# Kernel optimization log

Measured on AMD Instinct MI355X. Metric: run time of the kernel, lower is better.

Reference implementation:

```python
import jax, jax.numpy as jnp
import numpy as np

H, Dh, D = 12, 64, 8          # heads, head dim, depth slices
DS = Dh // D                   # per-depth slice dim = 8
EPS = 1e-6
MAW_STRENGTH = 0.15
ALPHA = 1.0 + 10.0 * MAW_STRENGTH  # 2.5


def _min_max_norm(v, eps=1e-12):
    vmin = v.min(axis=-1, keepdims=True)
    vmax = v.max(axis=-1, keepdims=True)
    return (v - vmin) / jnp.maximum(vmax - vmin, eps)


def setup_inputs() -> dict:
    key = jax.random.key(0)
    ks = jax.random.split(key, 8)
    B, L, E = 2, 768, H * Dh
    s = 0.02
    return {
        "hidden_states": jax.random.normal(ks[0], (B, L, E), jnp.float32),
        "attention_mask": jnp.zeros((B, L), jnp.float32),  # additive mask
        "Wq": jax.random.normal(ks[1], (E, E), jnp.float32) * s,
        "bq": jnp.zeros((E,), jnp.float32),
        "Wk": jax.random.normal(ks[2], (E, E), jnp.float32) * s,
        "bk": jnp.zeros((E,), jnp.float32),
        "Wv": jax.random.normal(ks[3], (E, E), jnp.float32) * s,
        "bv": jnp.zeros((E,), jnp.float32),
    }


def reference(hidden_states, attention_mask, Wq, bq, Wk, bk, Wv, bv):
    B, L, E = hidden_states.shape
    # projections -> [B, H, L, Dh]
    q = (hidden_states @ Wq + bq).reshape(B, L, H, Dh).transpose(0, 2, 1, 3)
    k = (hidden_states @ Wk + bk).reshape(B, L, H, Dh).transpose(0, 2, 1, 3)
    v = (hidden_states @ Wv + bv).reshape(B, L, H, Dh).transpose(0, 2, 1, 3)

    # depth-wise expansion: split head dim into D slices of size DS
    qd = q.reshape(B, H, L, D, DS)
    kd = k.reshape(B, H, L, D, DS)
    scores = jnp.einsum("bhqds,bhkds->bhdqk", qd, kd) / jnp.sqrt(jnp.float32(DS))
    # additive mask [B, Lk] -> [B, 1, 1, 1, Lk]
    scores = scores + attention_mask[:, None, None, None, :]
    attn = jax.nn.softmax(scores, axis=-1)  # [B, H, D, Lq, Lk]

    # statistical depth gating (mode='stat')
    var_k = jnp.var(attn, axis=-1, ddof=1).mean(axis=(1, 3))          # [B, D]
    max_k = attn.max(axis=-1).mean(axis=(1, 3))                        # [B, D]
    p = jnp.clip(attn, EPS, None)
    ent = (-p * jnp.log(p)).sum(axis=-1).mean(axis=(1, 3))             # [B, D]
    hhi = (attn * attn).sum(axis=-1).mean(axis=(1, 3))                 # [B, D]

    score = (0.5 * _min_max_norm(var_k) + 0.3 * _min_max_norm(max_k)
             + 0.2 * _min_max_norm(hhi) - 0.4 * _min_max_norm(ent))
    weights = jax.nn.softmax(ALPHA * score, axis=-1)                   # [B, D]

    # depth compression -> [B, H, Lq, Lk]
    attn4 = jnp.einsum("bhdqk,bd->bhqk", attn, weights)
    ctx = jnp.einsum("bhqk,bhkd->bhqd", attn4, v)                      # [B, H, L, Dh]
    ctx = ctx.transpose(0, 2, 1, 3).reshape(B, L, H * Dh)
    return ctx, attn4
```

## Files before the change

kernel.cpp:

```cpp
#include <hip/hip_runtime.h>

#define BATCH 2
#define L_SEQ 768
#define NH 12
#define DH 64
#define ND 8
#define EMB 768
#define RSQRT8 0.35355339059327373f

#define OFF_Q    0
#define OFF_K    1179648
#define OFF_V    2359296
#define OFF_L    3538944
#define OFF_PART 3686400
#define OFF_P2   6045696
#define OFF_W    6046464

__global__ __launch_bounds__(256) void k1_qkv(
    const float* __restrict__ hs,
    const float* __restrict__ Wq, const float* __restrict__ bq,
    const float* __restrict__ Wk, const float* __restrict__ bk,
    const float* __restrict__ Wv, const float* __restrict__ bvp,
    float* __restrict__ qw, float* __restrict__ kw, float* __restrict__ vw)
{
    __shared__ float AsT[64][68];
    __shared__ float Bs[64][68];
    const int tid = threadIdx.x;
    const int tx = tid & 15, ty = tid >> 4;
    const int bx = blockIdx.x, by = blockIdx.y, gz = blockIdx.z;
    const float* W    = (gz == 0) ? Wq : (gz == 1 ? Wk : Wv);
    const float* bias = (gz == 0) ? bq : (gz == 1 ? bk : bvp);
    float* dst        = (gz == 0) ? qw : (gz == 1 ? kw : vw);

    const int ldc = tx * 4;

    float acc[4][4];
#pragma unroll
    for (int i = 0; i < 4; i++)
#pragma unroll
        for (int j = 0; j < 4; j++) acc[i][j] = 0.f;

    for (int k0 = 0; k0 < EMB; k0 += 64) {
        __syncthreads();
#pragma unroll
        for (int i = 0; i < 4; i++) {
            int r = ty + 16 * i;
            float4 a = *(const float4*)&hs[(size_t)(by * 64 + r) * EMB + k0 + ldc];
            AsT[ldc + 0][r] = a.x; AsT[ldc + 1][r] = a.y;
            AsT[ldc + 2][r] = a.z; AsT[ldc + 3][r] = a.w;
            *(float4*)&Bs[r][ldc] =
                *(const float4*)&W[(size_t)(k0 + r) * EMB + bx * 64 + ldc];
        }
        __syncthreads();
#pragma unroll 8
        for (int kk = 0; kk < 64; kk++) {
            float av[4], bb[4];
            *(float4*)av = *(const float4*)&AsT[kk][ty * 4];
            *(float4*)bb = *(const float4*)&Bs[kk][tx * 4];
#pragma unroll
            for (int i = 0; i < 4; i++)
#pragma unroll
                for (int j = 0; j < 4; j++)
                    acc[i][j] = fmaf(av[i], bb[j], acc[i][j]);
        }
    }

#pragma unroll
    for (int i = 0; i < 4; i++) {
        int m = by * 64 + ty * 4 + i;
        int b2 = m / L_SEQ, l = m % L_SEQ;
        float o[4];
#pragma unroll
        for (int j = 0; j < 4; j++) o[j] = acc[i][j] + bias[bx * 64 + tx * 4 + j];
        *(float4*)&dst[((size_t)(b2 * NH + bx) * L_SEQ + l) * DH + tx * 4] = *(float4*)o;
    }
}

__global__ __launch_bounds__(256) void k2_stats(
    const float* __restrict__ qw, const float* __restrict__ kw,
    const float* __restrict__ mask, float* __restrict__ part)
{
    __shared__ float k_lds[64 * 64];
    __shared__ float m_lds[64];
    const int tid = threadIdx.x;
    const int lane = tid & 63, w = tid >> 6;
    const int qr = lane >> 3, d = lane & 7;
    const int lb = (blockIdx.x & 7) * 144 + (blockIdx.x >> 3);
    const int kq = lb & 3;
    const int t2 = lb >> 2;
    const int bh = t2 / 12;
    const int q0 = (t2 % 12) * 64;
    const int b = bh / NH;
    const int qw0 = q0 + w * 16;

    float qf[2][8];
#pragma unroll
    for (int qq = 0; qq < 2; qq++) {
        const float* qp = &qw[((size_t)bh * L_SEQ + qw0 + qr + qq * 8) * DH + d * 8];
        *(float4*)&qf[qq][0] = *(const float4*)qp;
        *(float4*)&qf[qq][4] = *(const float4*)(qp + 4);
    }
    float S[2] = {0.f, 0.f}, T2[2] = {0.f, 0.f}, SL[2] = {0.f, 0.f};
    float M[2] = {-1e30f, -1e30f};

    const int kb0 = kq * 192;
    for (int c = 0; c < 3; c++) {
        const int kb = kb0 + c * 64;
        __syncthreads();
        {
            const float* src = &kw[((size_t)bh * L_SEQ + kb) * DH];
#pragma unroll
            for (int i = 0; i < 4; i++) {
                int f = tid + 256 * i;
                *(float4*)&k_lds[f * 4] = *(const float4*)&src[f * 4];
            }
            if (tid < 64) m_lds[tid] = mask[b * L_SEQ + kb + tid];
        }
        __syncthreads();
#pragma unroll 4
        for (int kk = 0; kk < 64; kk++) {
            float kv[8];
            *(float4*)&kv[0] = *(const float4*)&k_lds[kk * 64 + d * 8];
            *(float4*)&kv[4] = *(const float4*)&k_lds[kk * 64 + d * 8 + 4];
            float mval = m_lds[kk];
#pragma unroll
            for (int qq = 0; qq < 2; qq++) {
                float s = 0.f;
#pragma unroll
                for (int t = 0; t < 8; t++) s = fmaf(qf[qq][t], kv[t], s);
                s = fmaf(s, RSQRT8, mval);
                float e = __expf(s);
                S[qq] += e;
                T2[qq] = fmaf(e, e, T2[qq]);
                SL[qq] = fmaf(s, e, SL[qq]);
                M[qq] = fmaxf(M[qq], s);
            }
        }
    }
#pragma unroll
    for (int qq = 0; qq < 2; qq++) {
        int q = qw0 + qr + qq * 8;
        size_t base = (size_t)(bh * 8 + d) * 16;
        part[(base + 0 + kq) * 768 + q] = S[qq];
        part[(base + 4 + kq) * 768 + q] = T2[qq];
        part[(base + 8 + kq) * 768 + q] = SL[qq];
        part[(base + 12 + kq) * 768 + q] = M[qq];
    }
}

__global__ __launch_bounds__(256) void k3_reduce(
    const float* __restrict__ part, float* __restrict__ linv,
    float* __restrict__ part2)
{
    const int bdh = blockIdx.x;
    const int bd = bdh / 12, h = bdh % 12;
    const int b = bd >> 3, d = bd & 7;
    const int bh = b * NH + h;
    const int tid = threadIdx.x;
    const int lane = tid & 63, wave = tid >> 6;
    const size_t base = (size_t)(bh * 8 + d) * 16;
    float acc[4] = {0.f, 0.f, 0.f, 0.f};

    for (int q = tid; q < 768; q += 256) {
        float Sv = 0.f, T2v = 0.f, SLv = 0.f, Mv = -1e30f;
#pragma unroll
        for (int kq = 0; kq < 4; kq++) {
            Sv  += part[(base + 0 + kq) * 768 + q];
            T2v += part[(base + 4 + kq) * 768 + q];
            SLv += part[(base + 8 + kq) * 768 + q];
            Mv = fmaxf(Mv, part[(base + 12 + kq) * 768 + q]);
        }
        float inv = 1.0f / Sv;
        linv[((size_t)bh * 768 + q) * 8 + d] = inv;
        float hhi = T2v * inv * inv;
        float maxp = __expf(Mv) * inv;
        float ent = __logf(Sv) - SLv * inv;
        float var = (hhi - (1.0f / 768.0f)) * (1.0f / 767.0f);
        acc[0] += var; acc[1] += maxp; acc[2] += ent; acc[3] += hhi;
    }
    __shared__ float red[4][4];
#pragma unroll
    for (int st = 0; st < 4; st++) {
        float a = acc[st];
#pragma unroll
        for (int off = 32; off > 0; off >>= 1) a += __shfl_xor(a, off, 64);
        acc[st] = a;
    }
    if (lane == 0) {
#pragma unroll
        for (int st = 0; st < 4; st++) red[wave][st] = acc[st];
    }
    __syncthreads();
    if (tid == 0) {
#pragma unroll
        for (int st = 0; st < 4; st++)
            part2[(size_t)(bd * 12 + h) * 4 + st] =
                red[0][st] + red[1][st] + red[2][st] + red[3][st];
    }
}

__global__ __launch_bounds__(64) void k3_weights(
    const float* __restrict__ part2, float* __restrict__ wgt)
{
    __shared__ float stats_l[64];
    const int tid = threadIdx.x;
    {
        const int bd = tid >> 2, st = tid & 3;
        float s = 0.f;
#pragma unroll
        for (int h = 0; h < 12; h++) s += part2[(size_t)(bd * 12 + h) * 4 + st];
        stats_l[tid] = s * (1.0f / 9216.0f);
    }
    __syncthreads();
    if (tid == 0) {
        for (int b = 0; b < BATCH; b++) {
            float v[4][8];
            for (int st = 0; st < 4; st++)
                for (int d = 0; d < 8; d++) v[st][d] = stats_l[(b * 8 + d) * 4 + st];
            float nrm[4][8];
            for (int st = 0; st < 4; st++) {
                float mn = v[st][0], mx = v[st][0];
                for (int d = 1; d < 8; d++) { mn = fminf(mn, v[st][d]); mx = fmaxf(mx, v[st][d]); }
                float rng = fmaxf(mx - mn, 1e-12f);
                for (int d = 0; d < 8; d++) nrm[st][d] = (v[st][d] - mn) / rng;
            }
            float sc[8];
            for (int d = 0; d < 8; d++)
                sc[d] = 0.5f * nrm[0][d] + 0.3f * nrm[1][d] + 0.2f * nrm[3][d] - 0.4f * nrm[2][d];
            float m = 2.5f * sc[0];
            for (int d = 1; d < 8; d++) m = fmaxf(m, 2.5f * sc[d]);
            float e8[8]; float ssum = 0.f;
            for (int d = 0; d < 8; d++) { e8[d] = __expf(2.5f * sc[d] - m); ssum += e8[d]; }
            for (int d = 0; d < 8; d++) wgt[b * ND + d] = e8[d] / ssum;
        }
    }
}

__global__ __launch_bounds__(256, 4) void k45_fused(
    const float* __restrict__ qw, const float* __restrict__ kw,
    const float* __restrict__ vw, const float* __restrict__ mask,
    const float* __restrict__ linv, const float* __restrict__ wgt,
    float* __restrict__ out_a4, float* __restrict__ out_ctx)
{
    __shared__ float smem[4][64 * 20];
    const int tid = threadIdx.x;
    const int lane = tid & 63, w = tid >> 6;
    const int lb = (blockIdx.x & 7) * 144 + (blockIdx.x >> 3);
    const int bh = lb / 48;
    const int q0 = (lb % 48) * 16;
    const int b = bh / NH, h = bh % NH;
    const int qg = lane >> 4;
    const int dhl = lane & 15;

    const float* kbase = &kw[(size_t)bh * L_SEQ * DH];
    const float* vbase = &vw[(size_t)bh * L_SEQ * DH];
    const float* qtile = &qw[((size_t)bh * L_SEQ + q0) * DH];
    const float* ltile = &linv[((size_t)bh * L_SEQ + q0) * 8];

    float wv[8];
#pragma unroll
    for (int d = 0; d < 8; d++) wv[d] = wgt[b * ND + d];

    float acc[4][4];
#pragma unroll
    for (int i = 0; i < 4; i++)
#pragma unroll
        for (int j = 0; j < 4; j++) acc[i][j] = 0.f;

    float* sm = &smem[w][0];

    for (int c = 0; c < 3; c++) {
        const int kb = (w * 3 + c) * 64;
        const int krow = kb + lane;

        float kv[64];
        {
            const float* kp = &kbase[(size_t)krow * DH];
#pragma unroll
            for (int t = 0; t < 16; t++)
                *(float4*)&kv[t * 4] = *(const float4*)&kp[t * 4];
        }
        const float mval = mask[b * L_SEQ + krow];

#pragma unroll 2
        for (int q = 0; q < 16; q++) {
            const float* qp = &qtile[(size_t)q * DH];
            const float* lp = &ltile[(size_t)q * 8];
            float sd[8];
#pragma unroll
            for (int d = 0; d < 8; d++) sd[d] = 0.f;
#pragma unroll
            for (int d = 0; d < 8; d++)
#pragma unroll
                for (int t = 0; t < 8; t++)
                    sd[d] = fmaf(qp[d * 8 + t], kv[d * 8 + t], sd[d]);
            float a4v = 0.f;
#pragma unroll
            for (int d = 0; d < 8; d++) {
                float sv = fmaf(sd[d], RSQRT8, mval);
                a4v = fmaf(wv[d] * lp[d], __expf(sv), a4v);
            }
            out_a4[((size_t)bh * L_SEQ + q0 + q) * L_SEQ + krow] = a4v;
            sm[lane * 20 + q] = a4v;
        }

        const float* vrow = &vbase[(size_t)kb * DH + dhl * 4];
#pragma unroll 8
        for (int k = 0; k < 64; k++) {
            float av[4];
            *(float4*)av = *(const float4*)&sm[k * 20 + qg * 4];
            float4 vv = *(const float4*)&vrow[(size_t)k * DH];
#pragma unroll
            for (int i = 0; i < 4; i++) {
                acc[i][0] = fmaf(av[i], vv.x, acc[i][0]);
                acc[i][1] = fmaf(av[i], vv.y, acc[i][1]);
                acc[i][2] = fmaf(av[i], vv.z, acc[i][2]);
                acc[i][3] = fmaf(av[i], vv.w, acc[i][3]);
            }
        }
    }

#pragma unroll
    for (int i = 0; i < 4; i++)
        *(float4*)&sm[(qg * 4 + i) * 68 + dhl * 4] = *(float4*)&acc[i][0];
    __syncthreads();
    {
        const int q = tid >> 4;
        const int dh4 = (tid & 15) * 4;
        float r[4] = {0.f, 0.f, 0.f, 0.f};
#pragma unroll
        for (int ww = 0; ww < 4; ww++) {
            const float* s2 = &smem[ww][q * 68 + dh4];
#pragma unroll
            for (int j = 0; j < 4; j++) r[j] += s2[j];
        }
        *(float4*)&out_ctx[((size_t)b * L_SEQ + q0 + q) * EMB + h * DH + dh4] =
            *(float4*)r;
    }
}

extern "C" void kernel_launch(void* const* d_in, const int* in_sizes, int n_in,
                              void* d_out, int out_size, void* d_ws, size_t ws_size,
                              hipStream_t stream)
{
    const float* hs   = (const float*)d_in[0];
    const float* mask = (const float*)d_in[1];
    const float* Wq   = (const float*)d_in[2];
    const float* bq   = (const float*)d_in[3];
    const float* Wk   = (const float*)d_in[4];
    const float* bk   = (const float*)d_in[5];
    const float* Wv   = (const float*)d_in[6];
    const float* bv   = (const float*)d_in[7];

    float* ws = (float*)d_ws;
    float* qw    = ws + OFF_Q;
    float* kw    = ws + OFF_K;
    float* vw    = ws + OFF_V;
    float* linv  = ws + OFF_L;
    float* part  = ws + OFF_PART;
    float* part2 = ws + OFF_P2;
    float* wgt   = ws + OFF_W;

    float* out_ctx = (float*)d_out;
    float* out_a4  = (float*)d_out + (size_t)BATCH * L_SEQ * EMB;

    k1_qkv<<<dim3(12, 24, 3), 256, 0, stream>>>(hs, Wq, bq, Wk, bk, Wv, bv, qw, kw, vw);
    k2_stats<<<dim3(1152), 256, 0, stream>>>(qw, kw, mask, part);
    k3_reduce<<<dim3(192), 256, 0, stream>>>(part, linv, part2);
    k3_weights<<<dim3(1), 64, 0, stream>>>(part2, wgt);
    k45_fused<<<dim3(1152), 256, 0, stream>>>(qw, kw, vw, mask, linv, wgt,
                                              out_a4, out_ctx);
}
```

Before: 317.3 us.

## Rewrite QKV GEMM with register-held rows and prefetch K tiles in stats kernel

The QKV projection kernel drops its LDS-tiled 64x64 GEMM. Instead, each lane holds one hidden-state row chunk of 64 floats in registers and reads 8 weight columns per wave as wave-uniform scalar loads. The launch becomes a 1D grid of 1728 blocks with an XCD-aware block remap, intended to avoid LDS traffic and barriers. The stats kernel now register-prefetches the next K tile and mask chunk while the current tile is computed, overlapping global loads with math. The tradeoff is heavy register pressure from the 64-float kv array, plus lower reuse because each block covers only 32 output columns, which raises global and scalar load traffic on the weights.

```diff
diff --git a/kernel.cpp b/kernel.cpp
--- a/kernel.cpp
+++ b/kernel.cpp
@@ -16,64 +16,59 @@
 #define OFF_P2   6045696
 #define OFF_W    6046464
 
-__global__ __launch_bounds__(256) void k1_qkv(
+__global__ __launch_bounds__(256, 4) void k1_qkv(
     const float* __restrict__ hs,
     const float* __restrict__ Wq, const float* __restrict__ bq,
     const float* __restrict__ Wk, const float* __restrict__ bk,
     const float* __restrict__ Wv, const float* __restrict__ bvp,
     float* __restrict__ qw, float* __restrict__ kw, float* __restrict__ vw)
 {
-    __shared__ float AsT[64][68];
-    __shared__ float Bs[64][68];
-    const int tid = threadIdx.x;
-    const int tx = tid & 15, ty = tid >> 4;
-    const int bx = blockIdx.x, by = blockIdx.y, gz = blockIdx.z;
+    const int tid = threadIdx.x;
+    const int lane = tid & 63;
+    const int lb = (blockIdx.x & 7) * 216 + (blockIdx.x >> 3);
+    const int gz = lb / 576;
+    const int r2 = lb % 576;
+    const int by = r2 / 24;
+    const int bx = r2 % 24;
+
     const float* W    = (gz == 0) ? Wq : (gz == 1 ? Wk : Wv);
     const float* bias = (gz == 0) ? bq : (gz == 1 ? bk : bvp);
     float* dst        = (gz == 0) ? qw : (gz == 1 ? kw : vw);
 
-    const int ldc = tx * 4;
-
-    float acc[4][4];
-#pragma unroll
-    for (int i = 0; i < 4; i++)
-#pragma unroll
-        for (int j = 0; j < 4; j++) acc[i][j] = 0.f;
-
-    for (int k0 = 0; k0 < EMB; k0 += 64) {
-        __syncthreads();
-#pragma unroll
-        for (int i = 0; i < 4; i++) {
-            int r = ty + 16 * i;
-            float4 a = *(const float4*)&hs[(size_t)(by * 64 + r) * EMB + k0 + ldc];
-            AsT[ldc + 0][r] = a.x; AsT[ldc + 1][r] = a.y;
-            AsT[ldc + 2][r] = a.z; AsT[ldc + 3][r] = a.w;
-            *(float4*)&Bs[r][ldc] =
-                *(const float4*)&W[(size_t)(k0 + r) * EMB + bx * 64 + ldc];
-        }
-        __syncthreads();
+    const int n0 = __builtin_amdgcn_readfirstlane(bx * 32 + (tid >> 6) * 8);
+
+    const int m = by * 64 + lane;
+    const int b2 = m / L_SEQ, l = m % L_SEQ;
+    const float* hsrow = &hs[(size_t)m * EMB];
+
+    float acc[8];
+#pragma unroll
+    for (int j = 0; j < 8; j++) acc[j] = 0.f;
+
+#pragma unroll 1
+    for (int c = 0; c < 12; c++) {
+        const int kb = c * 64;
+        float kv[64];
+#pragma unroll
+        for (int t = 0; t < 16; t++)
+            *(float4*)&kv[t * 4] = *(const float4*)&hsrow[kb + t * 4];
 #pragma unroll 8
         for (int kk = 0; kk < 64; kk++) {
-            float av[4], bb[4];
-            *(float4*)av = *(const float4*)&AsT[kk][ty * 4];
-            *(float4*)bb = *(const float4*)&Bs[kk][tx * 4];
-#pragma unroll
-            for (int i = 0; i < 4; i++)
-#pragma unroll
-                for (int j = 0; j < 4; j++)
-                    acc[i][j] = fmaf(av[i], bb[j], acc[i][j]);
-        }
-    }
-
-#pragma unroll
-    for (int i = 0; i < 4; i++) {
-        int m = by * 64 + ty * 4 + i;
-        int b2 = m / L_SEQ, l = m % L_SEQ;
-        float o[4];
-#pragma unroll
-        for (int j = 0; j < 4; j++) o[j] = acc[i][j] + bias[bx * 64 + tx * 4 + j];
-        *(float4*)&dst[((size_t)(b2 * NH + bx) * L_SEQ + l) * DH + tx * 4] = *(float4*)o;
-    }
+            const float* wr = &W[(size_t)(kb + kk) * EMB + n0];
+#pragma unroll
+            for (int j = 0; j < 8; j++)
+                acc[j] = fmaf(kv[kk], wr[j], acc[j]);
+        }
+    }
+
+    const int h = n0 >> 6;
+    const int dh0 = n0 & 63;
+    float o[8];
+#pragma unroll
+    for (int j = 0; j < 8; j++) o[j] = acc[j] + bias[n0 + j];
+    float* op = &dst[((size_t)(b2 * NH + h) * L_SEQ + l) * DH + dh0];
+    *(float4*)&op[0] = *(float4*)&o[0];
+    *(float4*)&op[4] = *(float4*)&o[4];
 }
 
 __global__ __launch_bounds__(256) void k2_stats(
@@ -104,19 +99,32 @@
     float M[2] = {-1e30f, -1e30f};
 
     const int kb0 = kq * 192;
+
+    float4 pk[4];
+    float pm = 0.f;
+    {
+        const float* src = &kw[((size_t)bh * L_SEQ + kb0) * DH];
+#pragma unroll
+        for (int i = 0; i < 4; i++) pk[i] = *(const float4*)&src[(tid + 256 * i) * 4];
+        if (tid < 64) pm = mask[b * L_SEQ + kb0 + tid];
+    }
+
     for (int c = 0; c < 3; c++) {
-        const int kb = kb0 + c * 64;
         __syncthreads();
         {
+#pragma unroll
+            for (int i = 0; i < 4; i++)
+                *(float4*)&k_lds[(tid + 256 * i) * 4] = pk[i];
+            if (tid < 64) m_lds[tid] = pm;
+        }
+        __syncthreads();
+        if (c < 2) {
+            const int kb = kb0 + (c + 1) * 64;
             const float* src = &kw[((size_t)bh * L_SEQ + kb) * DH];
 #pragma unroll
-            for (int i = 0; i < 4; i++) {
-                int f = tid + 256 * i;
-                *(float4*)&k_lds[f * 4] = *(const float4*)&src[f * 4];
-            }
-            if (tid < 64) m_lds[tid] = mask[b * L_SEQ + kb + tid];
-        }
-        __syncthreads();
+            for (int i = 0; i < 4; i++) pk[i] = *(const float4*)&src[(tid + 256 * i) * 4];
+            if (tid < 64) pm = mask[b * L_SEQ + kb + tid];
+        }
 #pragma unroll 4
         for (int kk = 0; kk < 64; kk++) {
             float kv[8];
@@ -364,7 +372,7 @@
     float* out_ctx = (float*)d_out;
     float* out_a4  = (float*)d_out + (size_t)BATCH * L_SEQ * EMB;
 
-    k1_qkv<<<dim3(12, 24, 3), 256, 0, stream>>>(hs, Wq, bq, Wk, bk, Wv, bv, qw, kw, vw);
+    k1_qkv<<<dim3(1728), 256, 0, stream>>>(hs, Wq, bq, Wk, bk, Wv, bv, qw, kw, vw);
     k2_stats<<<dim3(1152), 256, 0, stream>>>(qw, kw, mask, part);
     k3_reduce<<<dim3(192), 256, 0, stream>>>(part, linv, part2);
     k3_weights<<<dim3(1), 64, 0, stream>>>(part2, wgt);
```

After: 765.1 us. 141% more time.

## Drop LDS tiling in QKV GEMM and prefetch K tiles in stats kernel

Applied to the files above, without the earlier changes.

The QKV projection kernel no longer stages tiles through shared memory. Each thread reads its four hidden-state rows and the weight columns straight from global memory, relying on the cache, which removes the barriers and LDS traffic. The stats kernel now loads the next K chunk and mask into registers while the current chunk is being processed, overlapping global loads with compute. The cost is much more global and cache traffic in the GEMM, since no data is reused through LDS, plus extra register pressure in the stats kernel.

```diff
diff --git a/kernel.cpp b/kernel.cpp
--- a/kernel.cpp
+++ b/kernel.cpp
@@ -23,8 +23,6 @@
     const float* __restrict__ Wv, const float* __restrict__ bvp,
     float* __restrict__ qw, float* __restrict__ kw, float* __restrict__ vw)
 {
-    __shared__ float AsT[64][68];
-    __shared__ float Bs[64][68];
     const int tid = threadIdx.x;
     const int tx = tid & 15, ty = tid >> 4;
     const int bx = blockIdx.x, by = blockIdx.y, gz = blockIdx.z;
@@ -33,6 +31,11 @@
     float* dst        = (gz == 0) ? qw : (gz == 1 ? kw : vw);
 
     const int ldc = tx * 4;
+    const float* a0 = &hs[(size_t)(by * 64 + ty * 4 + 0) * EMB];
+    const float* a1 = &hs[(size_t)(by * 64 + ty * 4 + 1) * EMB];
+    const float* a2r = &hs[(size_t)(by * 64 + ty * 4 + 2) * EMB];
+    const float* a3 = &hs[(size_t)(by * 64 + ty * 4 + 3) * EMB];
+    const float* Wc = &W[bx * 64 + ldc];
 
     float acc[4][4];
 #pragma unroll
@@ -40,28 +43,23 @@
 #pragma unroll
         for (int j = 0; j < 4; j++) acc[i][j] = 0.f;
 
-    for (int k0 = 0; k0 < EMB; k0 += 64) {
-        __syncthreads();
-#pragma unroll
-        for (int i = 0; i < 4; i++) {
-            int r = ty + 16 * i;
-            float4 a = *(const float4*)&hs[(size_t)(by * 64 + r) * EMB + k0 + ldc];
-            AsT[ldc + 0][r] = a.x; AsT[ldc + 1][r] = a.y;
-            AsT[ldc + 2][r] = a.z; AsT[ldc + 3][r] = a.w;
-            *(float4*)&Bs[r][ldc] =
-                *(const float4*)&W[(size_t)(k0 + r) * EMB + bx * 64 + ldc];
-        }
-        __syncthreads();
-#pragma unroll 8
-        for (int kk = 0; kk < 64; kk++) {
-            float av[4], bb[4];
-            *(float4*)av = *(const float4*)&AsT[kk][ty * 4];
-            *(float4*)bb = *(const float4*)&Bs[kk][tx * 4];
+#pragma unroll 2
+    for (int k4 = 0; k4 < 192; k4++) {
+        const int kk = k4 * 4;
+        float a[4][4];
+        *(float4*)&a[0][0] = *(const float4*)&a0[kk];
+        *(float4*)&a[1][0] = *(const float4*)&a1[kk];
+        *(float4*)&a[2][0] = *(const float4*)&a2r[kk];
+        *(float4*)&a[3][0] = *(const float4*)&a3[kk];
+#pragma unroll
+        for (int u = 0; u < 4; u++) {
+            float b[4];
+            *(float4*)b = *(const float4*)&Wc[(size_t)(kk + u) * EMB];
 #pragma unroll
             for (int i = 0; i < 4; i++)
 #pragma unroll
                 for (int j = 0; j < 4; j++)
-                    acc[i][j] = fmaf(av[i], bb[j], acc[i][j]);
+                    acc[i][j] = fmaf(a[i][u], b[j], acc[i][j]);
         }
     }
 
@@ -104,19 +102,32 @@
     float M[2] = {-1e30f, -1e30f};
 
     const int kb0 = kq * 192;
+
+    float4 pk[4];
+    float pm = 0.f;
+    {
+        const float* src = &kw[((size_t)bh * L_SEQ + kb0) * DH];
+#pragma unroll
+        for (int i = 0; i < 4; i++) pk[i] = *(const float4*)&src[(tid + 256 * i) * 4];
+        if (tid < 64) pm = mask[b * L_SEQ + kb0 + tid];
+    }
+
     for (int c = 0; c < 3; c++) {
-        const int kb = kb0 + c * 64;
         __syncthreads();
         {
+#pragma unroll
+            for (int i = 0; i < 4; i++)
+                *(float4*)&k_lds[(tid + 256 * i) * 4] = pk[i];
+            if (tid < 64) m_lds[tid] = pm;
+        }
+        __syncthreads();
+        if (c < 2) {
+            const int kb = kb0 + (c + 1) * 64;
             const float* src = &kw[((size_t)bh * L_SEQ + kb) * DH];
 #pragma unroll
-            for (int i = 0; i < 4; i++) {
-                int f = tid + 256 * i;
-                *(float4*)&k_lds[f * 4] = *(const float4*)&src[f * 4];
-            }
-            if (tid < 64) m_lds[tid] = mask[b * L_SEQ + kb + tid];
-        }
-        __syncthreads();
+            for (int i = 0; i < 4; i++) pk[i] = *(const float4*)&src[(tid + 256 * i) * 4];
+            if (tid < 64) pm = mask[b * L_SEQ + kb + tid];
+        }
 #pragma unroll 4
         for (int kk = 0; kk < 64; kk++) {
             float kv[8];
```

New measurement: 418.5 us. 31.9% more time.
